# Kernel optimization log

Measured on AMD Instinct MI355X. Metric: run time of the kernel, lower is better.

## Reference

```python
import jax, jax.numpy as jnp
import numpy as np

N_NODES = 50000
N_EDGES = 800000
IN_DIM = 256
HID = 128
OUT = 128
HEADS = 2
EDGE_DIM = 2
NEG_SLOPE = 0.2


def _add_self_loops(src, dst, edge_attr, n):
    # PyG add_self_loops with fill_value='mean': self-loop edge_attr is the
    # mean of edge_attr over edges entering each node (0 if no in-edges).
    sums = jax.ops.segment_sum(edge_attr, dst, num_segments=n)
    cnt = jax.ops.segment_sum(jnp.ones((edge_attr.shape[0],), edge_attr.dtype), dst, num_segments=n)
    loop_attr = sums / jnp.maximum(cnt, 1.0)[:, None]
    ar = jnp.arange(n, dtype=src.dtype)
    return (jnp.concatenate([src, ar]), jnp.concatenate([dst, ar]),
            jnp.concatenate([edge_attr, loop_attr], axis=0))


def _gat_conv(x, src, dst, edge_attr, W, att_src, att_dst, We, att_e, bias, H, C):
    n = x.shape[0]
    xh = (x @ W).reshape(n, H, C)                      # [N,H,C]
    a_src = jnp.sum(xh * att_src, axis=-1)             # [N,H]
    a_dst = jnp.sum(xh * att_dst, axis=-1)             # [N,H]
    eh = (edge_attr @ We).reshape(-1, H, C)            # [E,H,C]
    a_e = jnp.sum(eh * att_e, axis=-1)                 # [E,H]
    logits = jax.nn.leaky_relu(a_src[src] + a_dst[dst] + a_e, NEG_SLOPE)
    # segment softmax over destination node
    m = jax.ops.segment_max(logits, dst, num_segments=n)
    m = jnp.where(jnp.isfinite(m), m, 0.0)
    ex = jnp.exp(logits - m[dst])
    denom = jax.ops.segment_sum(ex, dst, num_segments=n)
    alpha = ex / (denom[dst] + 1e-16)                  # [E,H]
    msg = xh[src] * alpha[:, :, None]                  # [E,H,C]
    out = jax.ops.segment_sum(msg, dst, num_segments=n)  # [N,H,C]
    return out.reshape(n, H * C) + bias


def setup_inputs() -> dict:
    key = jax.random.key(0)
    ks = jax.random.split(key, 16)
    s = 0.05
    inp = {
        "x": jax.random.normal(ks[0], (N_NODES, IN_DIM), jnp.float32),
        "edge_index": jax.random.randint(ks[1], (2, N_EDGES), 0, N_NODES, jnp.int32),
        "edge_attr": jax.random.normal(ks[2], (N_EDGES, EDGE_DIM), jnp.float32),
        # conv1: heads=2
        "W1": jax.random.normal(ks[3], (IN_DIM, HEADS * HID), jnp.float32) * s,
        "att_src1": jax.random.normal(ks[4], (HEADS, HID), jnp.float32) * s,
        "att_dst1": jax.random.normal(ks[5], (HEADS, HID), jnp.float32) * s,
        "We1": jax.random.normal(ks[6], (EDGE_DIM, HEADS * HID), jnp.float32) * s,
        "att_e1": jax.random.normal(ks[7], (HEADS, HID), jnp.float32) * s,
        "b1": jnp.zeros((HEADS * HID,), jnp.float32),
        # conv2: heads=1
        "W2": jax.random.normal(ks[8], (HEADS * HID, OUT), jnp.float32) * s,
        "att_src2": jax.random.normal(ks[9], (1, OUT), jnp.float32) * s,
        "att_dst2": jax.random.normal(ks[10], (1, OUT), jnp.float32) * s,
        "We2": jax.random.normal(ks[11], (EDGE_DIM, OUT), jnp.float32) * s,
        "att_e2": jax.random.normal(ks[12], (1, OUT), jnp.float32) * s,
        "b2": jnp.zeros((OUT,), jnp.float32),
    }
    return inp


def reference(x, edge_index, edge_attr, W1, att_src1, att_dst1, We1, att_e1, b1,
              W2, att_src2, att_dst2, We2, att_e2, b2):
    src, dst = edge_index[0], edge_index[1]
    src, dst, ea = _add_self_loops(src, dst, edge_attr, x.shape[0])
    h = _gat_conv(x, src, dst, ea, W1, att_src1, att_dst1, We1, att_e1, b1, HEADS, HID)
    h = jax.nn.elu(h)
    out = _gat_conv(h, src, dst, ea, W2, att_src2, att_dst2, We2, att_e2, b2, 1, OUT)
    return out
```

## Files before the change

kernel.cpp:

```cpp
#include <hip/hip_runtime.h>
#include <math.h>

#define N_NODES 50000
#define N_EDGES 800000
#define EP (N_EDGES + N_NODES)
#define NEG_SLOPE 0.2f
#define SCAN_BLOCKS ((N_NODES + 255) / 256)

typedef __attribute__((ext_vector_type(8))) short bf16x8;
typedef __attribute__((ext_vector_type(4))) float f32x4;

__device__ __forceinline__ unsigned short f2bf(float f) {
  unsigned u = __float_as_uint(f);
  unsigned r = (u + 0x7FFFu + ((u >> 16) & 1u)) >> 16;
  return (unsigned short)r;
}
__device__ __forceinline__ float bf2f(unsigned short b) {
  return __uint_as_float(((unsigned)b) << 16);
}

__global__ void fill_u32(unsigned* p, unsigned v, int n) {
  int i = blockIdx.x * blockDim.x + threadIdx.x;
  if (i < n) p[i] = v;
}

__global__ void rank_pass(const int* __restrict__ ei, int* __restrict__ cnt,
                          int* __restrict__ rank) {
  int e = blockIdx.x * blockDim.x + threadIdx.x;
  if (e >= N_EDGES) return;
  rank[e] = atomicAdd(&cnt[ei[N_EDGES + e]], 1);
}

__global__ void block_sums(const int* __restrict__ cnt, int* __restrict__ bsum) {
  __shared__ int ws[4];
  int b = blockIdx.x;
  int i = b * 256 + threadIdx.x;
  int v = (i < N_NODES) ? (cnt[i] + 1) : 0;
  #pragma unroll
  for (int off = 32; off > 0; off >>= 1) v += __shfl_down(v, off);
  if ((threadIdx.x & 63) == 0) ws[threadIdx.x >> 6] = v;
  __syncthreads();
  if (threadIdx.x == 0) bsum[b] = ws[0] + ws[1] + ws[2] + ws[3];
}

__global__ void scan_bsum(const int* __restrict__ bsum, int* __restrict__ boff) {
  __shared__ int buf[2][256];
  int t = threadIdx.x;
  int v = (t < SCAN_BLOCKS) ? bsum[t] : 0;
  buf[0][t] = v;
  __syncthreads();
  int cur = 0;
  for (int off = 1; off < 256; off <<= 1) {
    int x = buf[cur][t];
    if (t >= off) x += buf[cur][t - off];
    buf[cur ^ 1][t] = x;
    cur ^= 1;
    __syncthreads();
  }
  boff[t] = buf[cur][t] - v;
}

__global__ void emit_rowptr(const int* __restrict__ cnt, const int* __restrict__ boff,
                            int* __restrict__ rowptr) {
  __shared__ int buf[2][256];
  int b = blockIdx.x;
  int t = threadIdx.x;
  int i = b * 256 + t;
  int v = (i < N_NODES) ? (cnt[i] + 1) : 0;
  buf[0][t] = v;
  __syncthreads();
  int cur = 0;
  for (int off = 1; off < 256; off <<= 1) {
    int x = buf[cur][t];
    if (t >= off) x += buf[cur][t - off];
    buf[cur ^ 1][t] = x;
    cur ^= 1;
    __syncthreads();
  }
  int incl = buf[cur][t];
  int base = boff[b];
  if (i < N_NODES) {
    rowptr[i] = base + incl - v;
    if (i == N_NODES - 1) rowptr[N_NODES] = base + incl;
  }
}

__global__ void scatter_pass(const int* __restrict__ ei, const float* __restrict__ ea,
                             const int* __restrict__ rowptr, const int* __restrict__ rank,
                             uint2* __restrict__ ecsr) {
  int e = blockIdx.x * blockDim.x + threadIdx.x;
  if (e >= N_EDGES) return;
  int d = ei[N_EDGES + e];
  int pos = rowptr[d] + rank[e];
  uint2 v;
  v.x = (unsigned)ei[e];
  v.y = (unsigned)f2bf(ea[2 * e]) | ((unsigned)f2bf(ea[2 * e + 1]) << 16);
  ecsr[pos] = v;
}

__global__ void lattr_fin(const int* __restrict__ rowptr, uint2* __restrict__ ecsr) {
  int n = blockIdx.x * blockDim.x + threadIdx.x;
  if (n >= N_NODES) return;
  int beg = rowptr[n], end = rowptr[n + 1];
  float s0 = 0.f, s1 = 0.f;
  for (int j = beg; j < end - 1; ++j) {
    unsigned p = ecsr[j].y;
    s0 += __uint_as_float(p << 16);
    s1 += __uint_as_float(p & 0xFFFF0000u);
  }
  float c = fmaxf((float)(end - 1 - beg), 1.0f);
  uint2 m;
  m.x = (unsigned)n;
  m.y = (unsigned)f2bf(s0 / c) | ((unsigned)f2bf(s1 / c) << 16);
  ecsr[end - 1] = m;
}

__global__ void prep_ae(const float* __restrict__ We1, const float* __restrict__ ae1,
                        const float* __restrict__ We2, const float* __restrict__ ae2,
                        float* __restrict__ Ae) {
  int b = blockIdx.x;
  int t = threadIdx.x;
  float s = 0.f;
  if (b < 4) {
    int d = b >> 1, h = b & 1;
    for (int c = t; c < 128; c += 64)
      s += We1[d * 256 + h * 128 + c] * ae1[h * 128 + c];
  } else {
    int d = b - 4;
    for (int c = t; c < 128; c += 64)
      s += We2[d * 128 + c] * ae2[c];
  }
  for (int off = 32; off > 0; off >>= 1) s += __shfl_down(s, off);
  if (t == 0) Ae[b] = s;
}

__global__ void bt_split(const float* __restrict__ W1, const float* __restrict__ W2,
                         unsigned short* __restrict__ b1h, unsigned short* __restrict__ b1l,
                         unsigned short* __restrict__ b2h, unsigned short* __restrict__ b2l) {
  int n = blockIdx.x;
  int k = threadIdx.x;
  float v; unsigned short* ph; unsigned short* pl; int idx;
  if (n < 256) { v = W1[k * 256 + n];       ph = b1h; pl = b1l; idx = n * 256 + k; }
  else         { v = W2[k * 128 + (n - 256)]; ph = b2h; pl = b2l; idx = (n - 256) * 256 + k; }
  unsigned short h = f2bf(v);
  ph[idx] = h;
  pl[idx] = f2bf(v - bf2f(h));
}

template <int H>
__global__ __launch_bounds__(256) void gemm_split(
    const float* __restrict__ A,
    const unsigned short* __restrict__ Bth, const unsigned short* __restrict__ Btl,
    unsigned short* __restrict__ C, int M, int N,
    const float* __restrict__ att_src, const float* __restrict__ att_dst,
    float* __restrict__ asrc, float* __restrict__ adst) {
  __shared__ __attribute__((aligned(16))) unsigned short As[2][64][40];
  __shared__ __attribute__((aligned(16))) unsigned short Bs[2][128][40];
  __shared__ float redS[2][64], redD[2][64];
  int bm = blockIdx.y * 64, bn = blockIdx.x * 128;
  int tid = threadIdx.x;
  int l = tid & 63;
  int wid = tid >> 6;
  int wr = wid >> 1, wc = wid & 1;
  int rr = l & 15, kc = l >> 4;

  f32x4 acc[2][4];
  #pragma unroll
  for (int i = 0; i < 2; ++i)
    #pragma unroll
    for (int j = 0; j < 4; ++j)
      acc[i][j] = (f32x4){0.f, 0.f, 0.f, 0.f};

  int ar = tid >> 2, ac = tid & 3;
  int gm = bm + ar;

  for (int kt = 0; kt < 8; ++kt) {
    int k0 = kt * 32;
    float4 f0 = {0.f, 0.f, 0.f, 0.f}, f1 = f0;
    if (gm < M) {
      f0 = *(const float4*)(A + (size_t)gm * 256 + k0 + ac * 8);
      f1 = *(const float4*)(A + (size_t)gm * 256 + k0 + ac * 8 + 4);
    }
    float f[8] = {f0.x, f0.y, f0.z, f0.w, f1.x, f1.y, f1.z, f1.w};
    unsigned hw[4], lw[4];
    #pragma unroll
    for (int q = 0; q < 4; ++q) {
      unsigned short ha = f2bf(f[2 * q]),  hb = f2bf(f[2 * q + 1]);
      unsigned short la = f2bf(f[2 * q] - bf2f(ha)), lb = f2bf(f[2 * q + 1] - bf2f(hb));
      hw[q] = (unsigned)ha | ((unsigned)hb << 16);
      lw[q] = (unsigned)la | ((unsigned)lb << 16);
    }
    *(uint4*)&As[0][ar][ac * 8] = make_uint4(hw[0], hw[1], hw[2], hw[3]);
    *(uint4*)&As[1][ar][ac * 8] = make_uint4(lw[0], lw[1], lw[2], lw[3]);
    #pragma unroll
    for (int p = 0; p < 2; ++p) {
      int id = tid + p * 256;
      int nn = id >> 2, cc = id & 3;
      *(uint4*)&Bs[0][nn][cc * 8] = *(const uint4*)(Bth + (size_t)(bn + nn) * 256 + k0 + cc * 8);
      *(uint4*)&Bs[1][nn][cc * 8] = *(const uint4*)(Btl + (size_t)(bn + nn) * 256 + k0 + cc * 8);
    }
    __syncthreads();
    bf16x8 ah[2], alo[2], bh[4], bl[4];
    #pragma unroll
    for (int i = 0; i < 2; ++i) {
      ah[i]  = *(const bf16x8*)&As[0][wr * 32 + i * 16 + rr][kc * 8];
      alo[i] = *(const bf16x8*)&As[1][wr * 32 + i * 16 + rr][kc * 8];
    }
    #pragma unroll
    for (int j = 0; j < 4; ++j) {
      bh[j] = *(const bf16x8*)&Bs[0][wc * 64 + j * 16 + rr][kc * 8];
      bl[j] = *(const bf16x8*)&Bs[1][wc * 64 + j * 16 + rr][kc * 8];
    }
    #pragma unroll
    for (int i = 0; i < 2; ++i)
      #pragma unroll
      for (int j = 0; j < 4; ++j) {
        acc[i][j] = __builtin_amdgcn_mfma_f32_16x16x32_bf16(ah[i],  bh[j], acc[i][j], 0, 0, 0);
        acc[i][j] = __builtin_amdgcn_mfma_f32_16x16x32_bf16(ah[i],  bl[j], acc[i][j], 0, 0, 0);
        acc[i][j] = __builtin_amdgcn_mfma_f32_16x16x32_bf16(alo[i], bh[j], acc[i][j], 0, 0, 0);
      }
    __syncthreads();
  }

  #pragma unroll
  for (int i = 0; i < 2; ++i)
    #pragma unroll
    for (int reg = 0; reg < 4; ++reg) {
      int row = bm + wr * 32 + i * 16 + kc * 4 + reg;
      if (row < M) {
        #pragma unroll
        for (int j = 0; j < 4; ++j) {
          int col = bn + wc * 64 + j * 16 + rr;
          C[(size_t)row * N + col] = f2bf(acc[i][j][reg]);
        }
      }
    }

  int head = (H == 2) ? (bn >> 7) : 0;
  float ats[4], atd[4];
  #pragma unroll
  for (int j = 0; j < 4; ++j) {
    int colh = wc * 64 + j * 16 + rr;
    ats[j] = att_src[head * 128 + colh];
    atd[j] = att_dst[head * 128 + colh];
  }
  #pragma unroll
  for (int i = 0; i < 2; ++i)
    #pragma unroll
    for (int reg = 0; reg < 4; ++reg) {
      float sp = acc[i][0][reg] * ats[0] + acc[i][1][reg] * ats[1] +
                 acc[i][2][reg] * ats[2] + acc[i][3][reg] * ats[3];
      float dp = acc[i][0][reg] * atd[0] + acc[i][1][reg] * atd[1] +
                 acc[i][2][reg] * atd[2] + acc[i][3][reg] * atd[3];
      #pragma unroll
      for (int off = 1; off < 16; off <<= 1) {
        sp += __shfl_xor(sp, off);
        dp += __shfl_xor(dp, off);
      }
      if (rr == 0) {
        int row_local = wr * 32 + i * 16 + kc * 4 + reg;
        redS[wc][row_local] = sp;
        redD[wc][row_local] = dp;
      }
    }
  __syncthreads();
  if (tid < 64) {
    int row = bm + tid;
    if (row < M) {
      asrc[row * H + head] = redS[0][tid] + redS[1][tid];
      adst[row * H + head] = redD[0][tid] + redD[1][tid];
    }
  }
}

template <int H, int ACT>
__global__ __launch_bounds__(64)
void aggregate_fused(const unsigned short* __restrict__ xh, const float* __restrict__ asrc,
                     const float* __restrict__ adst, const uint2* __restrict__ ecsr,
                     const int* __restrict__ rowptr,
                     const float* __restrict__ Ae, int aeoff,
                     const float* __restrict__ bias, float* __restrict__ out) {
  constexpr int D = H * 128;
  constexpr int COLS = D / 64;
  __shared__ float exl[256][H];
  __shared__ int sl[256];
  int n = blockIdx.x;
  int t = threadIdx.x;
  int beg = rowptr[n], end = rowptr[n + 1];
  int hA = t & (H - 1);
  float adnA = adst[n * H + hA];
  float Ae0 = Ae[aeoff + hA], Ae1 = Ae[aeoff + H + hA];
  int hB = (H == 2) ? (t >> 5) : 0;
  float lsum = 0.f;
  float acc[4][COLS];
  #pragma unroll
  for (int q = 0; q < 4; ++q)
    #pragma unroll
    for (int c = 0; c < COLS; ++c) acc[q][c] = 0.f;

  for (int cbeg = beg; cbeg < end; cbeg += 256) {
    int cnt = min(256, end - cbeg);
    for (int idx = t; idx < cnt * H; idx += 64) {
      int j0 = (H == 2) ? (idx >> 1) : idx;
      uint2 ev = ecsr[cbeg + j0];
      int s = (int)ev.x;
      float ea0 = __uint_as_float(ev.y << 16);
      float ea1 = __uint_as_float(ev.y & 0xFFFF0000u);
      float lg = asrc[s * H + hA] + adnA + ea0 * Ae0 + ea1 * Ae1;
      lg = (lg > 0.f) ? lg : NEG_SLOPE * lg;
      float ex = __expf(lg);
      exl[j0][hA] = ex;
      if (hA == 0) sl[j0] = s;
      lsum += ex;
    }
    __syncthreads();
    int j = 0;
    for (; j + 8 <= cnt; j += 8) {
      #pragma unroll
      for (int q = 0; q < 8; ++q) {
        float e = exl[j + q][hB];
        int s = sl[j + q];
        if (COLS == 4) {
          uint2 u = *(const uint2*)(xh + (size_t)s * D + 4 * t);
          acc[q & 3][0] = fmaf(e, __uint_as_float(u.x << 16), acc[q & 3][0]);
          acc[q & 3][1] = fmaf(e, __uint_as_float(u.x & 0xFFFF0000u), acc[q & 3][1]);
          acc[q & 3][2] = fmaf(e, __uint_as_float(u.y << 16), acc[q & 3][2]);
          acc[q & 3][3] = fmaf(e, __uint_as_float(u.y & 0xFFFF0000u), acc[q & 3][3]);
        } else {
          unsigned u = *(const unsigned*)(xh + (size_t)s * D + 2 * t);
          acc[q & 3][0] = fmaf(e, __uint_as_float(u << 16), acc[q & 3][0]);
          acc[q & 3][1] = fmaf(e, __uint_as_float(u & 0xFFFF0000u), acc[q & 3][1]);
        }
      }
    }
    for (; j < cnt; ++j) {
      float e = exl[j][hB];
      int s = sl[j];
      if (COLS == 4) {
        uint2 u = *(const uint2*)(xh + (size_t)s * D + 4 * t);
        acc[0][0] = fmaf(e, __uint_as_float(u.x << 16), acc[0][0]);
        acc[0][1] = fmaf(e, __uint_as_float(u.x & 0xFFFF0000u), acc[0][1]);
        acc[0][2] = fmaf(e, __uint_as_float(u.y << 16), acc[0][2]);
        acc[0][3] = fmaf(e, __uint_as_float(u.y & 0xFFFF0000u), acc[0][3]);
      } else {
        unsigned u = *(const unsigned*)(xh + (size_t)s * D + 2 * t);
        acc[0][0] = fmaf(e, __uint_as_float(u << 16), acc[0][0]);
        acc[0][1] = fmaf(e, __uint_as_float(u & 0xFFFF0000u), acc[0][1]);
      }
    }
    __syncthreads();
  }

  #pragma unroll
  for (int off = H; off < 64; off <<= 1) lsum += __shfl_xor(lsum, off);
  float tot = (H == 2) ? __shfl(lsum, hB) : lsum;
  float inv = 1.0f / (tot + 1e-16f);

  float v[COLS];
  #pragma unroll
  for (int c = 0; c < COLS; ++c) {
    v[c] = fmaf(inv, (acc[0][c] + acc[1][c]) + (acc[2][c] + acc[3][c]),
                bias[COLS * t + c]);
    if (ACT) v[c] = (v[c] > 0.f) ? v[c] : expm1f(v[c]);
  }
  if (COLS == 4) {
    *(float4*)(out + (size_t)n * D + 4 * t) = make_float4(v[0], v[1], v[2], v[3]);
  } else {
    *(float2*)(out + (size_t)n * D + 2 * t) = make_float2(v[0], v[1]);
  }
}

extern "C" void kernel_launch(void* const* d_in, const int* in_sizes, int n_in,
                              void* d_out, int out_size, void* d_ws, size_t ws_size,
                              hipStream_t stream) {
  const float* x    = (const float*)d_in[0];
  const int*   ei   = (const int*)d_in[1];
  const float* ea   = (const float*)d_in[2];
  const float* W1   = (const float*)d_in[3];
  const float* as1  = (const float*)d_in[4];
  const float* ad1  = (const float*)d_in[5];
  const float* We1  = (const float*)d_in[6];
  const float* ae1  = (const float*)d_in[7];
  const float* b1   = (const float*)d_in[8];
  const float* W2   = (const float*)d_in[9];
  const float* as2  = (const float*)d_in[10];
  const float* ad2  = (const float*)d_in[11];
  const float* We2  = (const float*)d_in[12];
  const float* ae2  = (const float*)d_in[13];
  const float* b2   = (const float*)d_in[14];
  float* out = (float*)d_out;

  char* w = (char*)d_ws;
  size_t off = 0;
  auto alloc = [&](size_t bytes) -> void* {
    void* p = w + off;
    off = (off + bytes + 255) & ~(size_t)255;
    return p;
  };
  unsigned short* xhb   = (unsigned short*)alloc((size_t)N_NODES * 256 * 2);
  float*          hbuf  = (float*)alloc((size_t)N_NODES * 256 * 4);
  unsigned short* B1hi  = (unsigned short*)alloc(256 * 256 * 2);
  unsigned short* B1lo  = (unsigned short*)alloc(256 * 256 * 2);
  unsigned short* B2hi  = (unsigned short*)alloc(128 * 256 * 2);
  unsigned short* B2lo  = (unsigned short*)alloc(128 * 256 * 2);
  int*      rowptr   = (int*)alloc((N_NODES + 1) * 4);
  int*      cnt      = (int*)alloc(N_NODES * 4);
  int*      rank     = (int*)alloc((size_t)N_EDGES * 4);
  int*      bsum     = (int*)alloc(256 * 4);
  int*      boff     = (int*)alloc(256 * 4);
  uint2*    ecsr     = (uint2*)alloc((size_t)EP * 8);
  float*    asrc     = (float*)alloc(N_NODES * 2 * 4);
  float*    adst     = (float*)alloc(N_NODES * 2 * 4);
  float*    Ae       = (float*)alloc(16 * 4);

  auto cdiv = [](int a, int b) { return (a + b - 1) / b; };

  fill_u32<<<cdiv(N_NODES, 256), 256, 0, stream>>>((unsigned*)cnt, 0u, N_NODES);
  rank_pass<<<cdiv(N_EDGES, 256), 256, 0, stream>>>(ei, cnt, rank);
  block_sums<<<SCAN_BLOCKS, 256, 0, stream>>>(cnt, bsum);
  scan_bsum<<<1, 256, 0, stream>>>(bsum, boff);
  emit_rowptr<<<SCAN_BLOCKS, 256, 0, stream>>>(cnt, boff, rowptr);
  scatter_pass<<<cdiv(N_EDGES, 256), 256, 0, stream>>>(ei, ea, rowptr, rank, ecsr);
  lattr_fin<<<cdiv(N_NODES, 256), 256, 0, stream>>>(rowptr, ecsr);

  prep_ae<<<6, 64, 0, stream>>>(We1, ae1, We2, ae2, Ae);
  bt_split<<<384, 256, 0, stream>>>(W1, W2, B1hi, B1lo, B2hi, B2lo);

  gemm_split<2><<<dim3(2, cdiv(N_NODES, 64)), 256, 0, stream>>>(x, B1hi, B1lo, xhb, N_NODES, 256,
                                                                as1, ad1, asrc, adst);
  aggregate_fused<2, 1><<<N_NODES, 64, 0, stream>>>(xhb, asrc, adst, ecsr, rowptr,
                                                    Ae, 0, b1, hbuf);

  gemm_split<1><<<dim3(1, cdiv(N_NODES, 64)), 256, 0, stream>>>(hbuf, B2hi, B2lo, xhb, N_NODES, 128,
                                                                as2, ad2, asrc, adst);
  aggregate_fused<1, 0><<<N_NODES, 64, 0, stream>>>(xhb, asrc, adst, ecsr, rowptr,
                                                    Ae, 4, b2, out);
}
```

Baseline: 243.7 us.

## Pack four nodes per aggregate block, merge scan and prep kernels

The aggregate kernels now process four destination nodes per 256-thread block, one wavefront each, with per-wave LDS slices. Block-wide __syncthreads are replaced by a wave-local lgkmcnt wait. The separate block-offset scan is folded into emit_rowptr, where every block rescans the block sums itself. The self-loop attribute, weight split and attention-edge prep kernels are merged into one launch. The goal is fewer launches and less per-block scheduling overhead. The risk is correctness of the wave-level LDS synchronisation, and the larger blocks may change occupancy.

```diff
diff --git a/kernel.cpp b/kernel.cpp
--- a/kernel.cpp
+++ b/kernel.cpp
@@ -43,11 +43,12 @@
   if (threadIdx.x == 0) bsum[b] = ws[0] + ws[1] + ws[2] + ws[3];
 }
 
-__global__ void scan_bsum(const int* __restrict__ bsum, int* __restrict__ boff) {
+__global__ void emit_rowptr(const int* __restrict__ cnt, const int* __restrict__ bsum,
+                            int* __restrict__ rowptr) {
   __shared__ int buf[2][256];
-  int t = threadIdx.x;
-  int v = (t < SCAN_BLOCKS) ? bsum[t] : 0;
-  buf[0][t] = v;
+  int b = blockIdx.x, t = threadIdx.x;
+  int vb = (t < SCAN_BLOCKS) ? bsum[t] : 0;
+  buf[0][t] = vb;
   __syncthreads();
   int cur = 0;
   for (int off = 1; off < 256; off <<= 1) {
@@ -57,28 +58,21 @@
     cur ^= 1;
     __syncthreads();
   }
-  boff[t] = buf[cur][t] - v;
-}
-
-__global__ void emit_rowptr(const int* __restrict__ cnt, const int* __restrict__ boff,
-                            int* __restrict__ rowptr) {
-  __shared__ int buf[2][256];
-  int b = blockIdx.x;
-  int t = threadIdx.x;
+  int base = buf[cur][b] - ((b < SCAN_BLOCKS) ? bsum[b] : 0);
+  __syncthreads();
   int i = b * 256 + t;
   int v = (i < N_NODES) ? (cnt[i] + 1) : 0;
-  buf[0][t] = v;
+  buf[cur][t] = v;
   __syncthreads();
-  int cur = 0;
+  int c2 = cur;
   for (int off = 1; off < 256; off <<= 1) {
-    int x = buf[cur][t];
-    if (t >= off) x += buf[cur][t - off];
-    buf[cur ^ 1][t] = x;
-    cur ^= 1;
+    int x = buf[c2][t];
+    if (t >= off) x += buf[c2][t - off];
+    buf[c2 ^ 1][t] = x;
+    c2 ^= 1;
     __syncthreads();
   }
-  int incl = buf[cur][t];
-  int base = boff[b];
+  int incl = buf[c2][t];
   if (i < N_NODES) {
     rowptr[i] = base + incl - v;
     if (i == N_NODES - 1) rowptr[N_NODES] = base + incl;
@@ -98,53 +92,56 @@
   ecsr[pos] = v;
 }
 
-__global__ void lattr_fin(const int* __restrict__ rowptr, uint2* __restrict__ ecsr) {
-  int n = blockIdx.x * blockDim.x + threadIdx.x;
-  if (n >= N_NODES) return;
-  int beg = rowptr[n], end = rowptr[n + 1];
-  float s0 = 0.f, s1 = 0.f;
-  for (int j = beg; j < end - 1; ++j) {
-    unsigned p = ecsr[j].y;
-    s0 += __uint_as_float(p << 16);
-    s1 += __uint_as_float(p & 0xFFFF0000u);
-  }
-  float c = fmaxf((float)(end - 1 - beg), 1.0f);
-  uint2 m;
-  m.x = (unsigned)n;
-  m.y = (unsigned)f2bf(s0 / c) | ((unsigned)f2bf(s1 / c) << 16);
-  ecsr[end - 1] = m;
-}
-
-__global__ void prep_ae(const float* __restrict__ We1, const float* __restrict__ ae1,
-                        const float* __restrict__ We2, const float* __restrict__ ae2,
-                        float* __restrict__ Ae) {
+#define MISC_LATTR 196
+#define MISC_BT    384
+__global__ void prep_misc(const int* __restrict__ rowptr, uint2* __restrict__ ecsr,
+                          const float* __restrict__ W1, const float* __restrict__ W2,
+                          unsigned short* __restrict__ b1h, unsigned short* __restrict__ b1l,
+                          unsigned short* __restrict__ b2h, unsigned short* __restrict__ b2l,
+                          const float* __restrict__ ae1, const float* __restrict__ ae2,
+                          const float* __restrict__ We1, const float* __restrict__ We2,
+                          float* __restrict__ Ae) {
   int b = blockIdx.x;
   int t = threadIdx.x;
-  float s = 0.f;
-  if (b < 4) {
-    int d = b >> 1, h = b & 1;
-    for (int c = t; c < 128; c += 64)
-      s += We1[d * 256 + h * 128 + c] * ae1[h * 128 + c];
+  if (b < MISC_LATTR) {
+    int n = b * 256 + t;
+    if (n >= N_NODES) return;
+    int beg = rowptr[n], end = rowptr[n + 1];
+    float s0 = 0.f, s1 = 0.f;
+    for (int j = beg; j < end - 1; ++j) {
+      unsigned p = ecsr[j].y;
+      s0 += __uint_as_float(p << 16);
+      s1 += __uint_as_float(p & 0xFFFF0000u);
+    }
+    float c = fmaxf((float)(end - 1 - beg), 1.0f);
+    uint2 m;
+    m.x = (unsigned)n;
+    m.y = (unsigned)f2bf(s0 / c) | ((unsigned)f2bf(s1 / c) << 16);
+    ecsr[end - 1] = m;
+  } else if (b < MISC_LATTR + MISC_BT) {
+    int nb = b - MISC_LATTR;
+    float v; unsigned short* ph; unsigned short* pl; int idx;
+    if (nb < 256) { v = W1[t * 256 + nb];         ph = b1h; pl = b1l; idx = nb * 256 + t; }
+    else          { v = W2[t * 128 + (nb - 256)]; ph = b2h; pl = b2l; idx = (nb - 256) * 256 + t; }
+    unsigned short h = f2bf(v);
+    ph[idx] = h;
+    pl[idx] = f2bf(v - bf2f(h));
   } else {
-    int d = b - 4;
-    for (int c = t; c < 128; c += 64)
-      s += We2[d * 128 + c] * ae2[c];
-  }
-  for (int off = 32; off > 0; off >>= 1) s += __shfl_down(s, off);
-  if (t == 0) Ae[b] = s;
-}
-
-__global__ void bt_split(const float* __restrict__ W1, const float* __restrict__ W2,
-                         unsigned short* __restrict__ b1h, unsigned short* __restrict__ b1l,
-                         unsigned short* __restrict__ b2h, unsigned short* __restrict__ b2l) {
-  int n = blockIdx.x;
-  int k = threadIdx.x;
-  float v; unsigned short* ph; unsigned short* pl; int idx;
-  if (n < 256) { v = W1[k * 256 + n];       ph = b1h; pl = b1l; idx = n * 256 + k; }
-  else         { v = W2[k * 128 + (n - 256)]; ph = b2h; pl = b2l; idx = (n - 256) * 256 + k; }
-  unsigned short h = f2bf(v);
-  ph[idx] = h;
-  pl[idx] = f2bf(v - bf2f(h));
+    if (t >= 64) return;
+    int bb = b - (MISC_LATTR + MISC_BT);
+    float s = 0.f;
+    if (bb < 4) {
+      int d = bb >> 1, h = bb & 1;
+      for (int c = t; c < 128; c += 64)
+        s += We1[d * 256 + h * 128 + c] * ae1[h * 128 + c];
+    } else {
+      int d = bb - 4;
+      for (int c = t; c < 128; c += 64)
+        s += We2[d * 128 + c] * ae2[c];
+    }
+    for (int off = 32; off > 0; off >>= 1) s += __shfl_down(s, off);
+    if (t == 0) Ae[bb] = s;
+  }
 }
 
 template <int H>
@@ -274,7 +271,7 @@
 }
 
 template <int H, int ACT>
-__global__ __launch_bounds__(64)
+__global__ __launch_bounds__(256)
 void aggregate_fused(const unsigned short* __restrict__ xh, const float* __restrict__ asrc,
                      const float* __restrict__ adst, const uint2* __restrict__ ecsr,
                      const int* __restrict__ rowptr,
@@ -282,10 +279,12 @@
                      const float* __restrict__ bias, float* __restrict__ out) {
   constexpr int D = H * 128;
   constexpr int COLS = D / 64;
-  __shared__ float exl[256][H];
-  __shared__ int sl[256];
-  int n = blockIdx.x;
-  int t = threadIdx.x;
+  __shared__ float exl[4][256][H];
+  __shared__ int sl[4][256];
+  int wid = threadIdx.x >> 6;
+  int t = threadIdx.x & 63;
+  int n = blockIdx.x * 4 + wid;
+  if (n >= N_NODES) return;
   int beg = rowptr[n], end = rowptr[n + 1];
   int hA = t & (H - 1);
   float adnA = adst[n * H + hA];
@@ -309,17 +308,18 @@
       float lg = asrc[s * H + hA] + adnA + ea0 * Ae0 + ea1 * Ae1;
       lg = (lg > 0.f) ? lg : NEG_SLOPE * lg;
       float ex = __expf(lg);
-      exl[j0][hA] = ex;
-      if (hA == 0) sl[j0] = s;
+      exl[wid][j0][hA] = ex;
+      if (hA == 0) sl[wid][j0] = s;
       lsum += ex;
     }
-    __syncthreads();
+    asm volatile("s_waitcnt lgkmcnt(0)" ::: "memory");
+    __builtin_amdgcn_sched_barrier(0);
     int j = 0;
     for (; j + 8 <= cnt; j += 8) {
       #pragma unroll
       for (int q = 0; q < 8; ++q) {
-        float e = exl[j + q][hB];
-        int s = sl[j + q];
+        float e = exl[wid][j + q][hB];
+        int s = sl[wid][j + q];
         if (COLS == 4) {
           uint2 u = *(const uint2*)(xh + (size_t)s * D + 4 * t);
           acc[q & 3][0] = fmaf(e, __uint_as_float(u.x << 16), acc[q & 3][0]);
@@ -334,8 +334,8 @@
       }
     }
     for (; j < cnt; ++j) {
-      float e = exl[j][hB];
-      int s = sl[j];
+      float e = exl[wid][j][hB];
+      int s = sl[wid][j];
       if (COLS == 4) {
         uint2 u = *(const uint2*)(xh + (size_t)s * D + 4 * t);
         acc[0][0] = fmaf(e, __uint_as_float(u.x << 16), acc[0][0]);
@@ -348,7 +348,7 @@
         acc[0][1] = fmaf(e, __uint_as_float(u & 0xFFFF0000u), acc[0][1]);
       }
     }
-    __syncthreads();
+    asm volatile("" ::: "memory");
   }
 
   #pragma unroll
@@ -407,7 +407,6 @@
   int*      cnt      = (int*)alloc(N_NODES * 4);
   int*      rank     = (int*)alloc((size_t)N_EDGES * 4);
   int*      bsum     = (int*)alloc(256 * 4);
-  int*      boff     = (int*)alloc(256 * 4);
   uint2*    ecsr     = (uint2*)alloc((size_t)EP * 8);
   float*    asrc     = (float*)alloc(N_NODES * 2 * 4);
   float*    adst     = (float*)alloc(N_NODES * 2 * 4);
@@ -418,21 +417,19 @@
   fill_u32<<<cdiv(N_NODES, 256), 256, 0, stream>>>((unsigned*)cnt, 0u, N_NODES);
   rank_pass<<<cdiv(N_EDGES, 256), 256, 0, stream>>>(ei, cnt, rank);
   block_sums<<<SCAN_BLOCKS, 256, 0, stream>>>(cnt, bsum);
-  scan_bsum<<<1, 256, 0, stream>>>(bsum, boff);
-  emit_rowptr<<<SCAN_BLOCKS, 256, 0, stream>>>(cnt, boff, rowptr);
+  emit_rowptr<<<SCAN_BLOCKS, 256, 0, stream>>>(cnt, bsum, rowptr);
   scatter_pass<<<cdiv(N_EDGES, 256), 256, 0, stream>>>(ei, ea, rowptr, rank, ecsr);
-  lattr_fin<<<cdiv(N_NODES, 256), 256, 0, stream>>>(rowptr, ecsr);
-
-  prep_ae<<<6, 64, 0, stream>>>(We1, ae1, We2, ae2, Ae);
-  bt_split<<<384, 256, 0, stream>>>(W1, W2, B1hi, B1lo, B2hi, B2lo);
+  prep_misc<<<MISC_LATTR + MISC_BT + 6, 256, 0, stream>>>(rowptr, ecsr, W1, W2,
+                                                          B1hi, B1lo, B2hi, B2lo,
+                                                          ae1, ae2, We1, We2, Ae);
 
   gemm_split<2><<<dim3(2, cdiv(N_NODES, 64)), 256, 0, stream>>>(x, B1hi, B1lo, xhb, N_NODES, 256,
                                                                 as1, ad1, asrc, adst);
-  aggregate_fused<2, 1><<<N_NODES, 64, 0, stream>>>(xhb, asrc, adst, ecsr, rowptr,
-                                                    Ae, 0, b1, hbuf);
+  aggregate_fused<2, 1><<<cdiv(N_NODES, 4), 256, 0, stream>>>(xhb, asrc, adst, ecsr, rowptr,
+                                                              Ae, 0, b1, hbuf);
 
   gemm_split<1><<<dim3(1, cdiv(N_NODES, 64)), 256, 0, stream>>>(hbuf, B2hi, B2lo, xhb, N_NODES, 128,
                                                                 as2, ad2, asrc, adst);
-  aggregate_fused<1, 0><<<N_NODES, 64, 0, stream>>>(xhb, asrc, adst, ecsr, rowptr,
-                                                    Ae, 4, b2, out);
-}
+  aggregate_fused<1, 0><<<cdiv(N_NODES, 4), 256, 0, stream>>>(xhb, asrc, adst, ecsr, rowptr,
+                                                              Ae, 4, b2, out);
+}
```

After: 248.0 us. Within noise of the previous version (+1.8%).
